# Kernel tuning notes

Hardware: AMD Instinct MI355X
Metric: run time of the kernel (lower is better)

The kernel has to match this reference:

```python
import jax, jax.numpy as jnp
import numpy as np

D_MODEL, N_LATENTS, D_LATENT, N_HEADS = 2048, 512, 1024, 16
D_H = D_LATENT // N_HEADS
B, N = 4, 4096


def _split_heads(x):
    b, t, _ = x.shape
    return x.reshape(b, t, N_HEADS, D_H).transpose(0, 2, 1, 3)  # [B,H,T,d_h]


def _merge_heads(x):
    b, h, t, d = x.shape
    return x.transpose(0, 2, 1, 3).reshape(b, t, h * d)


def _apply_rope(x, cos, sin):
    b, h, s, d = x.shape
    xr = x.reshape(b, h, s, d // 2, 2)
    x1, x2 = xr[..., 0], xr[..., 1]
    c = cos[:s][None, None]  # [1,1,s,d/2]
    sn = sin[:s][None, None]
    o1 = x1 * c - x2 * sn
    o2 = x1 * sn + x2 * c
    return jnp.stack([o1, o2], axis=-1).reshape(b, h, s, d)


def _attn(Q, K, V, causal=False, padding_mask=None):
    scale = 1.0 / np.sqrt(D_H).astype(np.float32)
    scores = jnp.einsum('bhqd,bhkd->bhqk', Q, K) * scale
    if causal:
        sq, sk = Q.shape[-2], K.shape[-2]
        causal_mask = jnp.triu(jnp.ones((sq, sk), dtype=bool), k=1)
        scores = jnp.where(causal_mask[None, None], -jnp.inf, scores)
    if padding_mask is not None:
        scores = jnp.where(padding_mask[:, None, None, :], -jnp.inf, scores)
    w = jax.nn.softmax(scores, axis=-1)
    w = jnp.nan_to_num(w, nan=0.0)
    return jnp.einsum('bhqk,bhkd->bhqd', w, V)


def setup_inputs() -> dict:
    key = jax.random.key(0)
    ks = jax.random.split(key, 10)
    x = jax.random.normal(ks[0], (B, N, D_MODEL), dtype=jnp.float32)
    # real RoPE cache (head_dim = D_H)
    half = D_H // 2
    inv_freq = 1.0 / (10000.0 ** (jnp.arange(half, dtype=jnp.float32) / half))
    angles = jnp.arange(N, dtype=jnp.float32)[:, None] * inv_freq[None, :]
    cos, sin = jnp.cos(angles), jnp.sin(angles)
    padding_mask = jnp.zeros((B, N), dtype=bool)
    s = 0.02
    L = jax.random.normal(ks[1], (N_LATENTS, D_LATENT), jnp.float32) * (D_LATENT ** -0.5)
    Wq_lat = jax.random.normal(ks[2], (D_LATENT, D_LATENT), jnp.float32) * s
    Wk_in = jax.random.normal(ks[3], (D_MODEL, D_LATENT), jnp.float32) * s
    Wv_in = jax.random.normal(ks[4], (D_MODEL, D_LATENT), jnp.float32) * s
    Wq_in = jax.random.normal(ks[5], (D_MODEL, D_LATENT), jnp.float32) * s
    Wk_lat = jax.random.normal(ks[6], (D_LATENT, D_LATENT), jnp.float32) * s
    Wv_lat = jax.random.normal(ks[7], (D_LATENT, D_LATENT), jnp.float32) * s
    Wout = jax.random.normal(ks[8], (D_LATENT, D_MODEL), jnp.float32) * s
    return {"x": x, "cos": cos, "sin": sin, "padding_mask": padding_mask,
            "L": L, "Wq_lat": Wq_lat, "Wk_in": Wk_in, "Wv_in": Wv_in,
            "Wq_in": Wq_in, "Wk_lat": Wk_lat, "Wv_lat": Wv_lat, "Wout": Wout}


def reference(x, cos, sin, padding_mask, L, Wq_lat, Wk_in, Wv_in, Wq_in, Wk_lat, Wv_lat, Wout):
    b = x.shape[0]
    Lb = jnp.broadcast_to(L[None], (b, N_LATENTS, D_LATENT))
    # stage 1: latents query inputs (causal + padding)
    Q = _split_heads(Lb @ Wq_lat)
    K = _apply_rope(_split_heads(x @ Wk_in), cos, sin)
    V = _split_heads(x @ Wv_in)
    z = _merge_heads(_attn(Q, K, V, causal=True, padding_mask=padding_mask))
    # stage 2: latent self-attention
    Ql = _split_heads(z @ Wq_lat)
    Kl = _split_heads(z @ Wk_lat)
    Vl = _split_heads(z @ Wv_lat)
    z2 = _merge_heads(_attn(Ql, Kl, Vl))
    # stage 3: inputs query latents
    Qx = _apply_rope(_split_heads(x @ Wq_in), cos, sin)
    Kz = _split_heads(z2 @ Wk_lat)
    Vz = _split_heads(z2 @ Wv_lat)
    x_latent = _merge_heads(_attn(Qx, Kz, Vz))
    return x_latent @ Wout
```

## Files before the change

kernel.cpp:

```cpp
#include <hip/hip_runtime.h>
#include <math.h>

#define D_MODEL 2048
#define N_LAT   512
#define D_LATENT 1024
#define N_HEADS 16
#define D_H 64
#define BATCH 4
#define SEQ 4096

typedef __attribute__((ext_vector_type(4))) float f32x4;
typedef __attribute__((ext_vector_type(8))) short short8;

__device__ inline ushort f2bf(float f) {
    uint u = __float_as_uint(f);
    uint r = (u + 0x7fffu + ((u >> 16) & 1u)) >> 16;
    return (ushort)r;
}
__device__ inline float bf2f(ushort h) { return __uint_as_float((uint)h << 16); }
__device__ inline uint pk(ushort a, ushort b) { return (uint)a | ((uint)b << 16); }

__global__ __launch_bounds__(256) void pack_w(
    const float* __restrict__ W, ushort* __restrict__ Ph, ushort* __restrict__ Pl,
    int K, int N)
{
    __shared__ float T[64][65];
    const int k0 = blockIdx.x * 64, n0 = blockIdx.y * 64;
    const int tid = threadIdx.x;
    for (int i = tid; i < 64 * 16; i += 256) {
        int kl = i >> 4, nc = (i & 15) * 4;
        float4 v = *(const float4*)(W + (long)(k0 + kl) * N + n0 + nc);
        T[kl][nc] = v.x; T[kl][nc + 1] = v.y; T[kl][nc + 2] = v.z; T[kl][nc + 3] = v.w;
    }
    __syncthreads();
    const int nl = tid >> 2, kc = (tid & 3) * 16;
    ushort h[16], l[16];
#pragma unroll
    for (int j = 0; j < 16; ++j) {
        float v = T[kc + j][nl];
        ushort hb = f2bf(v);
        float r = v - bf2f(hb);
        h[j] = hb; l[j] = f2bf(r);
    }
    long o = (long)(n0 + nl) * K + k0 + kc;
    *(uint4*)(Ph + o)     = make_uint4(pk(h[0],h[1]), pk(h[2],h[3]), pk(h[4],h[5]), pk(h[6],h[7]));
    *(uint4*)(Ph + o + 8) = make_uint4(pk(h[8],h[9]), pk(h[10],h[11]), pk(h[12],h[13]), pk(h[14],h[15]));
    *(uint4*)(Pl + o)     = make_uint4(pk(l[0],l[1]), pk(l[2],l[3]), pk(l[4],l[5]), pk(l[6],l[7]));
    *(uint4*)(Pl + o + 8) = make_uint4(pk(l[8],l[9]), pk(l[10],l[11]), pk(l[12],l[13]), pk(l[14],l[15]));
}

__global__ __launch_bounds__(256) void split2bf(
    const float* __restrict__ X, ushort* __restrict__ H, ushort* __restrict__ L, long n)
{
    long i = ((long)blockIdx.x * 256 + threadIdx.x) * 4;
    const long stride = (long)gridDim.x * 1024;
    for (; i < n; i += stride) {
        float4 v = *(const float4*)(X + i);
        ushort h0 = f2bf(v.x), h1 = f2bf(v.y), h2 = f2bf(v.z), h3 = f2bf(v.w);
        ushort l0 = f2bf(v.x - bf2f(h0)), l1 = f2bf(v.y - bf2f(h1)),
               l2 = f2bf(v.z - bf2f(h2)), l3 = f2bf(v.w - bf2f(h3));
        uint2 hw; hw.x = pk(h0, h1); hw.y = pk(h2, h3);
        uint2 lw; lw.x = pk(l0, l1); lw.y = pk(l2, l3);
        *(uint2*)(H + i) = hw;
        *(uint2*)(L + i) = lw;
    }
}

__global__ __launch_bounds__(512) void gemm_mfma8(
    const ushort* __restrict__ Ah, const ushort* __restrict__ Al,
    const ushort* __restrict__ Bh0, const ushort* __restrict__ Bl0,
    const ushort* __restrict__ Bh1, const ushort* __restrict__ Bl1,
    const ushort* __restrict__ Bh2, const ushort* __restrict__ Bl2,
    float* __restrict__ C0, float* __restrict__ C1, float* __restrict__ C2,
    int N, int K, long asb, long csb, int nMt)
{
    __shared__ ushort sAh[128][40], sAl[128][40];
    __shared__ ushort sBh[128][40], sBl[128][40];

    const int gx = gridDim.x;
    const int nblk = gx * gridDim.y;
    int bl = blockIdx.y * gx + blockIdx.x;
    if ((nblk & 7) == 0)
        bl = (bl & 7) * (nblk >> 3) + (bl >> 3);
    const int bx = bl % gx;
    const int by = bl / gx;

    const int wsel = by / nMt, mt0 = by % nMt;
    const ushort* Bh = (wsel == 0) ? Bh0 : ((wsel == 1) ? Bh1 : Bh2);
    const ushort* Bl = (wsel == 0) ? Bl0 : ((wsel == 1) ? Bl1 : Bl2);
    float* C = (wsel == 0) ? C0 : ((wsel == 1) ? C1 : C2);
    Ah += (long)blockIdx.z * asb;
    Al += (long)blockIdx.z * asb;
    C  += (long)blockIdx.z * csb;
    const int row0 = mt0 * 128, col0 = bx * 128;
    const int tid = threadIdx.x;
    const int lane = tid & 63, w = tid >> 6;
    const int wm = (w >> 2) * 64;
    const int wn = (w & 3) * 32;

    f32x4 acc[4][2];
#pragma unroll
    for (int i = 0; i < 4; ++i)
#pragma unroll
        for (int j = 0; j < 2; ++j) acc[i][j] = (f32x4)0.f;

    const int srow = tid >> 2;
    const int scol = (tid & 3) * 8;
    const ushort* Ahp = Ah + (long)(row0 + srow) * K + scol;
    const ushort* Alp = Al + (long)(row0 + srow) * K + scol;
    const ushort* Bhp = Bh + (long)(col0 + srow) * K + scol;
    const ushort* Blp = Bl + (long)(col0 + srow) * K + scol;

    const int fr = lane & 15, fk = (lane >> 4) * 8;

    for (int k0 = 0; k0 < K; k0 += 32) {
        uint4 ra_h = *(const uint4*)(Ahp + k0);
        uint4 ra_l = *(const uint4*)(Alp + k0);
        uint4 rb_h = *(const uint4*)(Bhp + k0);
        uint4 rb_l = *(const uint4*)(Blp + k0);
        __syncthreads();
        *(uint4*)&sAh[srow][scol] = ra_h;
        *(uint4*)&sAl[srow][scol] = ra_l;
        *(uint4*)&sBh[srow][scol] = rb_h;
        *(uint4*)&sBl[srow][scol] = rb_l;
        __syncthreads();

        short8 bhf[2], blf[2];
#pragma unroll
        for (int nt = 0; nt < 2; ++nt) {
            bhf[nt] = *(const short8*)&sBh[wn + nt * 16 + fr][fk];
            blf[nt] = *(const short8*)&sBl[wn + nt * 16 + fr][fk];
        }
#pragma unroll
        for (int mt = 0; mt < 4; ++mt) {
            short8 ah = *(const short8*)&sAh[wm + mt * 16 + fr][fk];
            short8 al = *(const short8*)&sAl[wm + mt * 16 + fr][fk];
#pragma unroll
            for (int nt = 0; nt < 2; ++nt) {
                acc[mt][nt] = __builtin_amdgcn_mfma_f32_16x16x32_bf16(al, bhf[nt], acc[mt][nt], 0, 0, 0);
                acc[mt][nt] = __builtin_amdgcn_mfma_f32_16x16x32_bf16(ah, blf[nt], acc[mt][nt], 0, 0, 0);
                acc[mt][nt] = __builtin_amdgcn_mfma_f32_16x16x32_bf16(ah, bhf[nt], acc[mt][nt], 0, 0, 0);
            }
        }
    }

    const int cr = (lane >> 4) * 4, cc = lane & 15;
#pragma unroll
    for (int mt = 0; mt < 4; ++mt)
#pragma unroll
        for (int nt = 0; nt < 2; ++nt) {
            float* cp = C + (long)(row0 + wm + mt * 16 + cr) * N + col0 + wn + nt * 16 + cc;
#pragma unroll
            for (int i = 0; i < 4; ++i) cp[(long)i * N] = acc[mt][nt][i];
        }
}

__global__ __launch_bounds__(512) void gemm_mfma8_f32a(
    const float* __restrict__ A,
    const ushort* __restrict__ Bh0, const ushort* __restrict__ Bl0,
    const ushort* __restrict__ Bh1, const ushort* __restrict__ Bl1,
    float* __restrict__ C0, float* __restrict__ C1,
    int N, int K, long asb, long csb, int nMt)
{
    __shared__ ushort sAh[128][40], sAl[128][40];
    __shared__ ushort sBh[128][40], sBl[128][40];

    const int gx = gridDim.x;
    const int nblk = gx * gridDim.y;
    int bl = blockIdx.y * gx + blockIdx.x;
    if ((nblk & 7) == 0)
        bl = (bl & 7) * (nblk >> 3) + (bl >> 3);
    const int bx = bl % gx;
    const int by = bl / gx;

    const int wsel = by / nMt, mt0 = by % nMt;
    const ushort* Bh = (wsel == 0) ? Bh0 : Bh1;
    const ushort* Bl = (wsel == 0) ? Bl0 : Bl1;
    float* C = (wsel == 0) ? C0 : C1;
    A += (long)blockIdx.z * asb;
    C += (long)blockIdx.z * csb;
    const int row0 = mt0 * 128, col0 = bx * 128;
    const int tid = threadIdx.x;
    const int lane = tid & 63, w = tid >> 6;
    const int wm = (w >> 2) * 64;
    const int wn = (w & 3) * 32;

    f32x4 acc[4][2];
#pragma unroll
    for (int i = 0; i < 4; ++i)
#pragma unroll
        for (int j = 0; j < 2; ++j) acc[i][j] = (f32x4)0.f;

    const int srow = tid >> 2;
    const int scol = (tid & 3) * 8;
    const float*  Ap  = A  + (long)(row0 + srow) * K + scol;
    const ushort* Bhp = Bh + (long)(col0 + srow) * K + scol;
    const ushort* Blp = Bl + (long)(col0 + srow) * K + scol;

    const int fr = lane & 15, fk = (lane >> 4) * 8;

    for (int k0 = 0; k0 < K; k0 += 32) {
        float4 a0 = *(const float4*)(Ap + k0);
        float4 a1 = *(const float4*)(Ap + k0 + 4);
        uint4 rb_h = *(const uint4*)(Bhp + k0);
        uint4 rb_l = *(const uint4*)(Blp + k0);
        uint4 wh, wl;
        {
            float v[8] = {a0.x, a0.y, a0.z, a0.w, a1.x, a1.y, a1.z, a1.w};
            ushort hh[8], ll[8];
#pragma unroll
            for (int j = 0; j < 8; ++j) {
                hh[j] = f2bf(v[j]);
                ll[j] = f2bf(v[j] - bf2f(hh[j]));
            }
            wh = make_uint4(pk(hh[0],hh[1]), pk(hh[2],hh[3]), pk(hh[4],hh[5]), pk(hh[6],hh[7]));
            wl = make_uint4(pk(ll[0],ll[1]), pk(ll[2],ll[3]), pk(ll[4],ll[5]), pk(ll[6],ll[7]));
        }
        __syncthreads();
        *(uint4*)&sAh[srow][scol] = wh;
        *(uint4*)&sAl[srow][scol] = wl;
        *(uint4*)&sBh[srow][scol] = rb_h;
        *(uint4*)&sBl[srow][scol] = rb_l;
        __syncthreads();

        short8 bhf[2], blf[2];
#pragma unroll
        for (int nt = 0; nt < 2; ++nt) {
            bhf[nt] = *(const short8*)&sBh[wn + nt * 16 + fr][fk];
            blf[nt] = *(const short8*)&sBl[wn + nt * 16 + fr][fk];
        }
#pragma unroll
        for (int mt = 0; mt < 4; ++mt) {
            short8 ah = *(const short8*)&sAh[wm + mt * 16 + fr][fk];
            short8 al = *(const short8*)&sAl[wm + mt * 16 + fr][fk];
#pragma unroll
            for (int nt = 0; nt < 2; ++nt) {
                acc[mt][nt] = __builtin_amdgcn_mfma_f32_16x16x32_bf16(al, bhf[nt], acc[mt][nt], 0, 0, 0);
                acc[mt][nt] = __builtin_amdgcn_mfma_f32_16x16x32_bf16(ah, blf[nt], acc[mt][nt], 0, 0, 0);
                acc[mt][nt] = __builtin_amdgcn_mfma_f32_16x16x32_bf16(ah, bhf[nt], acc[mt][nt], 0, 0, 0);
            }
        }
    }

    const int cr = (lane >> 4) * 4, cc = lane & 15;
#pragma unroll
    for (int mt = 0; mt < 4; ++mt)
#pragma unroll
        for (int nt = 0; nt < 2; ++nt) {
            float* cp = C + (long)(row0 + wm + mt * 16 + cr) * N + col0 + wn + nt * 16 + cc;
#pragma unroll
            for (int i = 0; i < 4; ++i) cp[(long)i * N] = acc[mt][nt][i];
        }
}

__global__ __launch_bounds__(256) void rope_f32(
    float* __restrict__ X, const float* __restrict__ cosT, const float* __restrict__ sinT,
    int S, int nb)
{
    long idx = (long)blockIdx.x * blockDim.x + threadIdx.x;
    long total = (long)nb * S * (D_LATENT / 2);
    if (idx >= total) return;
    int pair = (int)(idx & (D_LATENT / 2 - 1));
    long rs = idx >> 9;
    int s = (int)(rs % S);
    long b = rs / S;
    int h = pair >> 5, t = pair & 31;
    long base = (b * S + s) * (long)D_LATENT + h * D_H + 2 * t;
    float x1 = X[base], x2 = X[base + 1];
    float c = cosT[(long)s * 32 + t], sn = sinT[(long)s * 32 + t];
    X[base]     = x1 * c - x2 * sn;
    X[base + 1] = x1 * sn + x2 * c;
}

__global__ __launch_bounds__(256) void attn_mfma(
    const float* __restrict__ Q,
    const ushort* __restrict__ Kh, const ushort* __restrict__ Kl,
    const ushort* __restrict__ VTh, const ushort* __restrict__ VTl,
    ushort* __restrict__ Oh, ushort* __restrict__ Ol,
    long qbs, long kvbs, long obs)
{
    const int b = blockIdx.z, h = blockIdx.y;
    const int qb0 = blockIdx.x * 64;
    const float*  Qp  = Q   + (long)b * qbs + h * D_H;
    const ushort* Khp = Kh  + (long)b * kvbs + h * D_H;
    const ushort* Klp = Kl  + (long)b * kvbs + h * D_H;
    const ushort* VThp = VTh + (long)b * kvbs + (long)h * D_H * 512;
    const ushort* VTlp = VTl + (long)b * kvbs + (long)h * D_H * 512;
    ushort* Ohp = Oh + (long)b * obs + h * D_H;
    ushort* Olp = Ol + (long)b * obs + h * D_H;

    __shared__ ushort QVhs[64][72], QVls[64][72];
    __shared__ ushort Khs[64][72], Kls[64][72];
    __shared__ ushort Ps[4][16][72];

    const int tid = threadIdx.x;
    const int w = tid >> 6, lane = tid & 63;
    const int fr = lane & 15, g = lane >> 4, fk = g * 8;

    {
        const int q = tid >> 2, d0 = (tid & 3) * 16;
        const float* qrow = Qp + (long)(qb0 + q) * D_LATENT + d0;
#pragma unroll
        for (int c = 0; c < 4; ++c) {
            float4 v = *(const float4*)(qrow + 4 * c);
            ushort h0 = f2bf(v.x), h1 = f2bf(v.y), h2 = f2bf(v.z), h3 = f2bf(v.w);
            ushort l0 = f2bf(v.x - bf2f(h0)), l1 = f2bf(v.y - bf2f(h1)),
                   l2 = f2bf(v.z - bf2f(h2)), l3 = f2bf(v.w - bf2f(h3));
            uint2 hw; hw.x = pk(h0, h1); hw.y = pk(h2, h3);
            uint2 lw; lw.x = pk(l0, l1); lw.y = pk(l2, l3);
            *(uint2*)&QVhs[q][d0 + 4 * c] = hw;
            *(uint2*)&QVls[q][d0 + 4 * c] = lw;
        }
    }
    __syncthreads();

    const short8 qh0 = *(const short8*)&QVhs[w * 16 + fr][fk];
    const short8 qh1 = *(const short8*)&QVhs[w * 16 + fr][32 + fk];
    const short8 ql0 = *(const short8*)&QVls[w * 16 + fr][fk];
    const short8 ql1 = *(const short8*)&QVls[w * 16 + fr][32 + fk];

    f32x4 ot[4];
#pragma unroll
    for (int dt = 0; dt < 4; ++dt) ot[dt] = (f32x4)0.f;
    float mq = -1e30f, lq = 0.f;

    for (int kc = 0; kc < 512; kc += 64) {
        __syncthreads();
        {
            const int r = tid >> 2, cb = (tid & 3) * 16;
            const ushort* kh = Khp + (long)(kc + r) * D_LATENT + cb;
            const ushort* kl = Klp + (long)(kc + r) * D_LATENT + cb;
            const ushort* vh = VThp + (long)r * 512 + kc + cb;
            const ushort* vl = VTlp + (long)r * 512 + kc + cb;
            uint4 a0 = *(const uint4*)kh,       a1 = *(const uint4*)(kh + 8);
            uint4 b0 = *(const uint4*)kl,       b1 = *(const uint4*)(kl + 8);
            uint4 c0 = *(const uint4*)vh,       c1 = *(const uint4*)(vh + 8);
            uint4 d0v = *(const uint4*)vl,      d1v = *(const uint4*)(vl + 8);
            *(uint4*)&Khs[r][cb] = a0; *(uint4*)&Khs[r][cb + 8] = a1;
            *(uint4*)&Kls[r][cb] = b0; *(uint4*)&Kls[r][cb + 8] = b1;
            *(uint4*)&QVhs[r][cb] = c0; *(uint4*)&QVhs[r][cb + 8] = c1;
            *(uint4*)&QVls[r][cb] = d0v; *(uint4*)&QVls[r][cb + 8] = d1v;
        }
        __syncthreads();

        f32x4 sc[4];
#pragma unroll
        for (int t = 0; t < 4; ++t) {
            short8 kh0 = *(const short8*)&Khs[t * 16 + fr][fk];
            short8 kh1 = *(const short8*)&Khs[t * 16 + fr][32 + fk];
            short8 kl0 = *(const short8*)&Kls[t * 16 + fr][fk];
            short8 kl1 = *(const short8*)&Kls[t * 16 + fr][32 + fk];
            f32x4 a = (f32x4)0.f;
            a = __builtin_amdgcn_mfma_f32_16x16x32_bf16(kh0, ql0, a, 0, 0, 0);
            a = __builtin_amdgcn_mfma_f32_16x16x32_bf16(kh1, ql1, a, 0, 0, 0);
            a = __builtin_amdgcn_mfma_f32_16x16x32_bf16(kl0, qh0, a, 0, 0, 0);
            a = __builtin_amdgcn_mfma_f32_16x16x32_bf16(kl1, qh1, a, 0, 0, 0);
            a = __builtin_amdgcn_mfma_f32_16x16x32_bf16(kh0, qh0, a, 0, 0, 0);
            a = __builtin_amdgcn_mfma_f32_16x16x32_bf16(kh1, qh1, a, 0, 0, 0);
            sc[t] = a;
        }

        float cm = -1e30f;
#pragma unroll
        for (int t = 0; t < 4; ++t)
#pragma unroll
            for (int r = 0; r < 4; ++r) {
                sc[t][r] *= 0.125f;
                cm = fmaxf(cm, sc[t][r]);
            }
        cm = fmaxf(cm, __shfl_xor(cm, 16));
        cm = fmaxf(cm, __shfl_xor(cm, 32));
        const float mnew = fmaxf(mq, cm);
        const float alpha = __expf(mq - mnew);
        float tsum = 0.f;
#pragma unroll
        for (int t = 0; t < 4; ++t)
#pragma unroll
            for (int r = 0; r < 4; ++r) {
                float p = __expf(sc[t][r] - mnew);
                sc[t][r] = p;
                tsum += p;
            }
        tsum += __shfl_xor(tsum, 16);
        tsum += __shfl_xor(tsum, 32);
        lq = lq * alpha + tsum;
        mq = mnew;
#pragma unroll
        for (int dt = 0; dt < 4; ++dt) ot[dt] = ot[dt] * alpha;

#pragma unroll
        for (int t = 0; t < 4; ++t)
#pragma unroll
            for (int r = 0; r < 4; ++r)
                Ps[w][fr][t * 16 + g * 4 + r] = f2bf(sc[t][r]);

#pragma unroll
        for (int ks = 0; ks < 2; ++ks) {
            short8 bp = *(const short8*)&Ps[w][fr][ks * 32 + fk];
#pragma unroll
            for (int dt = 0; dt < 4; ++dt) {
                short8 avh = *(const short8*)&QVhs[dt * 16 + fr][ks * 32 + fk];
                short8 avl = *(const short8*)&QVls[dt * 16 + fr][ks * 32 + fk];
                ot[dt] = __builtin_amdgcn_mfma_f32_16x16x32_bf16(avh, bp, ot[dt], 0, 0, 0);
                ot[dt] = __builtin_amdgcn_mfma_f32_16x16x32_bf16(avl, bp, ot[dt], 0, 0, 0);
            }
        }
    }

    __syncthreads();
    const float inv = 1.0f / lq;
#pragma unroll
    for (int dt = 0; dt < 4; ++dt)
#pragma unroll
        for (int r = 0; r < 4; ++r) {
            float v = ot[dt][r] * inv;
            ushort hb = f2bf(v);
            Khs[w * 16 + fr][dt * 16 + g * 4 + r] = hb;
            Kls[w * 16 + fr][dt * 16 + g * 4 + r] = f2bf(v - bf2f(hb));
        }
    __syncthreads();
    {
        const int q = tid >> 2, d0 = (tid & 3) * 16;
        ushort* oh = Ohp + (long)(qb0 + q) * D_LATENT + d0;
        ushort* ol = Olp + (long)(qb0 + q) * D_LATENT + d0;
        *(uint4*)oh       = *(const uint4*)&Khs[q][d0];
        *(uint4*)(oh + 8) = *(const uint4*)&Khs[q][d0 + 8];
        *(uint4*)ol       = *(const uint4*)&Kls[q][d0];
        *(uint4*)(ol + 8) = *(const uint4*)&Kls[q][d0 + 8];
    }
}

#define ABQ 64
#define ABK 64
#define APAD 68

__global__ __launch_bounds__(256, 3) void attn_f32(
    const float* __restrict__ Q, const float* __restrict__ K, const float* __restrict__ V,
    ushort* __restrict__ Oh, ushort* __restrict__ Ol,
    int Sq, int Sk, long qbs, long kvbs, long obs, int causal)
{
    const int b = blockIdx.z, h = blockIdx.y;
    const int qb0 = blockIdx.x * ABQ;
    const float* Qp = Q + (long)b * qbs + h * D_H;
    const float* Kp = K + (long)b * kvbs + h * D_H;
    const float* Vp = V + (long)b * kvbs + h * D_H;
    ushort* Ohp = Oh + (long)b * obs + h * D_H;
    ushort* Olp = Ol + (long)b * obs + h * D_H;

    __shared__ float Qs[D_H][APAD];
    __shared__ float KPs[D_H][APAD];
    __shared__ float Vs[ABK][APAD];

    const int tid = threadIdx.x;
    const int tm = tid >> 4;
    const int tn = tid & 15;
    const int q4 = tm * 4, n4 = tn * 4;

    for (int i = tid; i < ABQ * 16; i += 256) {
        int q = i >> 4, d0 = (i & 15) * 4;
        float4 t = *(const float4*)(Qp + (long)(qb0 + q) * D_LATENT + d0);
        Qs[d0 + 0][q] = t.x; Qs[d0 + 1][q] = t.y; Qs[d0 + 2][q] = t.z; Qs[d0 + 3][q] = t.w;
    }

    float o[4][4], mq[4], lq[4];
#pragma unroll
    for (int i = 0; i < 4; ++i) {
        mq[i] = -1e30f; lq[i] = 0.f;
#pragma unroll
        for (int j = 0; j < 4; ++j) o[i][j] = 0.f;
    }

    const int kend = causal ? min(Sk, qb0 + ABQ) : Sk;

    for (int kc = 0; kc < kend; kc += ABK) {
        __syncthreads();
        for (int i = tid; i < ABK * 16; i += 256) {
            int k = i >> 4, d0 = (i & 15) * 4;
            float4 kt = *(const float4*)(Kp + (long)(kc + k) * D_LATENT + d0);
            KPs[d0 + 0][k] = kt.x; KPs[d0 + 1][k] = kt.y; KPs[d0 + 2][k] = kt.z; KPs[d0 + 3][k] = kt.w;
            float4 vt = *(const float4*)(Vp + (long)(kc + k) * D_LATENT + d0);
            *(float4*)&Vs[k][d0] = vt;
        }
        __syncthreads();

        float s[4][4];
#pragma unroll
        for (int qi = 0; qi < 4; ++qi)
#pragma unroll
            for (int kj = 0; kj < 4; ++kj) s[qi][kj] = 0.f;

#pragma unroll 4
        for (int d = 0; d < D_H; ++d) {
            float4 qv = *(const float4*)&Qs[d][q4];
            float4 kv = *(const float4*)&KPs[d][n4];
            float qa[4] = {qv.x, qv.y, qv.z, qv.w};
            float ka[4] = {kv.x, kv.y, kv.z, kv.w};
#pragma unroll
            for (int qi = 0; qi < 4; ++qi)
#pragma unroll
                for (int kj = 0; kj < 4; ++kj) s[qi][kj] += qa[qi] * ka[kj];
        }
        __syncthreads();

        const bool diag = (causal != 0) && (kc + ABK > qb0);
#pragma unroll
        for (int qi = 0; qi < 4; ++qi) {
            const int gq = qb0 + q4 + qi;
#pragma unroll
            for (int kj = 0; kj < 4; ++kj) {
                float sv = s[qi][kj] * 0.125f;
                if (diag && (kc + n4 + kj > gq)) sv = -1e30f;
                s[qi][kj] = sv;
            }
            float cm = fmaxf(fmaxf(s[qi][0], s[qi][1]), fmaxf(s[qi][2], s[qi][3]));
#pragma unroll
            for (int off = 8; off; off >>= 1) cm = fmaxf(cm, __shfl_xor(cm, off));
            const float mnew = fmaxf(mq[qi], cm);
            float ps = 0.f;
#pragma unroll
            for (int kj = 0; kj < 4; ++kj) {
                float p = __expf(s[qi][kj] - mnew);
                s[qi][kj] = p;
                ps += p;
            }
#pragma unroll
            for (int off = 8; off; off >>= 1) ps += __shfl_xor(ps, off);
            const float alpha = __expf(mq[qi] - mnew);
            lq[qi] = lq[qi] * alpha + ps;
            mq[qi] = mnew;
#pragma unroll
            for (int dj = 0; dj < 4; ++dj) o[qi][dj] *= alpha;
        }
#pragma unroll
        for (int kj = 0; kj < 4; ++kj)
            *(float4*)&KPs[n4 + kj][q4] = make_float4(s[0][kj], s[1][kj], s[2][kj], s[3][kj]);
        __syncthreads();

#pragma unroll 4
        for (int k = 0; k < ABK; ++k) {
            float4 pv = *(const float4*)&KPs[k][q4];
            float4 vv = *(const float4*)&Vs[k][n4];
            float pa[4] = {pv.x, pv.y, pv.z, pv.w};
            float va[4] = {vv.x, vv.y, vv.z, vv.w};
#pragma unroll
            for (int qi = 0; qi < 4; ++qi)
#pragma unroll
                for (int dj = 0; dj < 4; ++dj) o[qi][dj] += pa[qi] * va[dj];
        }
    }

#pragma unroll
    for (int qi = 0; qi < 4; ++qi) {
        const float inv = 1.0f / lq[qi];
        float v0 = o[qi][0] * inv, v1 = o[qi][1] * inv, v2 = o[qi][2] * inv, v3 = o[qi][3] * inv;
        ushort h0 = f2bf(v0), h1 = f2bf(v1), h2 = f2bf(v2), h3 = f2bf(v3);
        ushort l0 = f2bf(v0 - bf2f(h0)), l1 = f2bf(v1 - bf2f(h1)),
               l2 = f2bf(v2 - bf2f(h2)), l3 = f2bf(v3 - bf2f(h3));
        uint2 hw; hw.x = pk(h0, h1); hw.y = pk(h2, h3);
        uint2 lw; lw.x = pk(l0, l1); lw.y = pk(l2, l3);
        long off = (long)(qb0 + q4 + qi) * D_LATENT + n4;
        *(uint2*)(Ohp + off) = hw;
        *(uint2*)(Olp + off) = lw;
    }
}

extern "C" void kernel_launch(void* const* d_in, const int* in_sizes, int n_in,
                              void* d_out, int out_size, void* d_ws, size_t ws_size,
                              hipStream_t stream)
{
    const float* x     = (const float*)d_in[0];
    const float* cosT  = (const float*)d_in[1];
    const float* sinT  = (const float*)d_in[2];
    const float* L      = (const float*)d_in[4];
    const float* Wq_lat = (const float*)d_in[5];
    const float* Wk_in  = (const float*)d_in[6];
    const float* Wv_in  = (const float*)d_in[7];
    const float* Wq_in  = (const float*)d_in[8];
    const float* Wk_lat = (const float*)d_in[9];
    const float* Wv_lat = (const float*)d_in[10];
    const float* Wout   = (const float*)d_in[11];
    float* out = (float*)d_out;
    float* ws  = (float*)d_ws;
    ushort* wsu = (ushort*)d_ws;
    ushort* ob  = (ushort*)d_out;

    const long F  = 524288;
    const long UU = 1048576;
    if (ws_size < (size_t)47 * UU * 2) return;

    ushort *Po_h  = wsu + 0 * UU, *Po_l  = wsu + 2 * UU;
    ushort *Pqi_h = wsu + 4 * UU, *Pqi_l = wsu + 6 * UU;
    ushort *Pql_h = wsu + 8 * UU, *Pql_l = wsu + 9 * UU;
    ushort *Pki_h = wsu + 10 * UU, *Pki_l = wsu + 12 * UU;
    ushort *Pvi_h = wsu + 14 * UU, *Pvi_l = wsu + 16 * UU;
    ushort *Pkl_h = wsu + 18 * UU, *Pkl_l = wsu + 19 * UU;
    ushort *Pvl_h = wsu + 20 * UU, *Pvl_l = wsu + 21 * UU;
    float  *Q1 = ws + 31 * F;
    float  *K1 = ws + 32 * F, *V1 = ws + 36 * F;
    ushort *zh = wsu + 40 * UU, *zl = wsu + 42 * UU;
    float  *Ql = ws + 23 * F, *Kl = ws + 27 * F, *Vl = ws + 32 * F;
    ushort *Klh = wsu + 40 * UU, *Kll = wsu + 42 * UU;
    ushort *VlTh = wsu + 27 * UU, *VlTl = wsu + 29 * UU;
    ushort *z2h = wsu + 36 * UU, *z2l = wsu + 38 * UU;
    float  *Kz = ws + 23 * F, *Vz = ws + 27 * F;
    ushort *Kzh = wsu + 31 * UU, *Kzl = wsu + 33 * UU;
    ushort *VzTh = wsu + 35 * UU, *VzTl = wsu + 37 * UU;
    ushort *xl23h = wsu + 22 * UU;
    ushort *xl23l = wsu + 39 * UU;

    float  *Qx = out;
    ushort *xl01h = ob + 32 * UU, *xl01l = ob + 40 * UU;

    dim3 blk(256), blk5(512);
    const long SB = (long)N_LAT * D_LATENT;
    const long XB = (long)SEQ * D_MODEL;
    const long QB = (long)SEQ * D_LATENT;

    pack_w<<<dim3(16, 32), blk, 0, stream>>>(Wout,   Po_h,  Po_l,  1024, 2048);
    pack_w<<<dim3(32, 16), blk, 0, stream>>>(Wq_in,  Pqi_h, Pqi_l, 2048, 1024);
    pack_w<<<dim3(16, 16), blk, 0, stream>>>(Wq_lat, Pql_h, Pql_l, 1024, 1024);
    pack_w<<<dim3(32, 16), blk, 0, stream>>>(Wk_in,  Pki_h, Pki_l, 2048, 1024);
    pack_w<<<dim3(32, 16), blk, 0, stream>>>(Wv_in,  Pvi_h, Pvi_l, 2048, 1024);
    pack_w<<<dim3(16, 16), blk, 0, stream>>>(Wk_lat, Pkl_h, Pkl_l, 1024, 1024);
    pack_w<<<dim3(16, 16), blk, 0, stream>>>(Wv_lat, Pvl_h, Pvl_l, 1024, 1024);

    gemm_mfma8_f32a<<<dim3(8, 4, 1), blk5, 0, stream>>>(
        L, Pql_h, Pql_l, nullptr, nullptr,
        Q1, nullptr, 1024, 1024, 0L, 0L, 4);
    gemm_mfma8_f32a<<<dim3(8, 8, BATCH), blk5, 0, stream>>>(
        x, Pki_h, Pki_l, Pvi_h, Pvi_l,
        K1, V1, 1024, 2048, (long)SEQ * D_MODEL, SB, 4);
    {
        long total = (long)BATCH * N_LAT * (D_LATENT / 2);
        rope_f32<<<dim3((unsigned)((total + 255) / 256)), blk, 0, stream>>>(K1, cosT, sinT, N_LAT, BATCH);
    }
    attn_f32<<<dim3(N_LAT / ABQ, N_HEADS, BATCH), blk, 0, stream>>>(
        Q1, K1, V1, zh, zl, N_LAT, N_LAT, 0L, SB, SB, 1);

    gemm_mfma8<<<dim3(8, 12, BATCH), blk5, 0, stream>>>(
        zh, zl, Pql_h, Pql_l, Pkl_h, Pkl_l, Pvl_h, Pvl_l,
        Ql, Kl, Vl, 1024, 1024, SB, SB, 4);
    split2bf<<<dim3(512), blk, 0, stream>>>(Kl, Klh, Kll, 4L * SB);
    for (int b = 0; b < BATCH; ++b)
        pack_w<<<dim3(8, 16), blk, 0, stream>>>(
            Vl + (long)b * SB, VlTh + (long)b * SB, VlTl + (long)b * SB, 512, 1024);
    attn_mfma<<<dim3(N_LAT / 64, N_HEADS, BATCH), blk, 0, stream>>>(
        Ql, Klh, Kll, VlTh, VlTl, z2h, z2l, SB, SB, SB);

    gemm_mfma8<<<dim3(8, 8, BATCH), blk5, 0, stream>>>(
        z2h, z2l, Pkl_h, Pkl_l, Pvl_h, Pvl_l, nullptr, nullptr,
        Kz, Vz, nullptr, 1024, 1024, SB, SB, 4);
    split2bf<<<dim3(512), blk, 0, stream>>>(Kz, Kzh, Kzl, 4L * SB);
    for (int b = 0; b < BATCH; ++b)
        pack_w<<<dim3(8, 16), blk, 0, stream>>>(
            Vz + (long)b * SB, VzTh + (long)b * SB, VzTl + (long)b * SB, 512, 1024);

    gemm_mfma8_f32a<<<dim3(8, 64, 1), blk5, 0, stream>>>(
        x, Pqi_h, Pqi_l, nullptr, nullptr,
        Qx, nullptr, 1024, 2048, 0L, 0L, 64);
    gemm_mfma8_f32a<<<dim3(8, 64, 1), blk5, 0, stream>>>(
        x + 2L * XB, Pqi_h, Pqi_l, nullptr, nullptr,
        Qx + 2L * QB, nullptr, 1024, 2048, 0L, 0L, 64);
    {
        long total = (long)BATCH * SEQ * (D_LATENT / 2);
        rope_f32<<<dim3((unsigned)((total + 255) / 256)), blk, 0, stream>>>(Qx, cosT, sinT, SEQ, BATCH);
    }
    attn_mfma<<<dim3(SEQ / 64, N_HEADS, 2), blk, 0, stream>>>(
        Qx, Kzh, Kzl, VzTh, VzTl, xl01h, xl01l, QB, SB, QB);
    attn_mfma<<<dim3(SEQ / 64, N_HEADS, 2), blk, 0, stream>>>(
        Qx + 2L * QB, Kzh + 2L * SB, Kzl + 2L * SB, VzTh + 2L * SB, VzTl + 2L * SB,
        xl23h, xl23l, QB, SB, QB);
    gemm_mfma8<<<dim3(16, 64, 1), blk5, 0, stream>>>(
        xl01h, xl01l, Po_h, Po_l, nullptr, nullptr, nullptr, nullptr,
        out, nullptr, nullptr, 2048, 1024, 0L, 0L, 64);
    gemm_mfma8<<<dim3(16, 64, 1), blk5, 0, stream>>>(
        xl23h, xl23l, Po_h, Po_l, nullptr, nullptr, nullptr, nullptr,
        out + 2L * SEQ * D_MODEL, nullptr, nullptr, 2048, 1024, 0L, 0L, 64);
}
```

Before: 1.048 ms.

## Use MFMA attention for causal stage and smaller GEMM tiles for latent GEMMs

The scalar fp32 stage-1 attention is replaced by the MFMA split-bf16 attention kernel, which gains a causal flag with diagonal masking and early loop termination. K1 is split into bf16 hi/lo parts and V1 is transposed to feed it. The GEMM kernels are templated on M-tile size, so the small latent GEMMs run with 64-row tiles for more blocks, and the two Qx GEMM launches are merged into one. The costs are extra split and pack passes, and lower per-block reuse in the smaller-tile GEMMs.

After: 967.6 us. 7.7% less time.

```diff
diff --git a/kernel.cpp b/kernel.cpp
--- a/kernel.cpp
+++ b/kernel.cpp
@@ -66,6 +66,7 @@
     }
 }
 
+template<int MT>
 __global__ __launch_bounds__(512) void gemm_mfma8(
     const ushort* __restrict__ Ah, const ushort* __restrict__ Al,
     const ushort* __restrict__ Bh0, const ushort* __restrict__ Bl0,
@@ -74,7 +75,8 @@
     float* __restrict__ C0, float* __restrict__ C1, float* __restrict__ C2,
     int N, int K, long asb, long csb, int nMt)
 {
-    __shared__ ushort sAh[128][40], sAl[128][40];
+    constexpr int BM = MT * 32;
+    __shared__ ushort sAh[BM][40], sAl[BM][40];
     __shared__ ushort sBh[128][40], sBl[128][40];
 
     const int gx = gridDim.x;
@@ -92,37 +94,47 @@
     Ah += (long)blockIdx.z * asb;
     Al += (long)blockIdx.z * asb;
     C  += (long)blockIdx.z * csb;
-    const int row0 = mt0 * 128, col0 = bx * 128;
+    const int row0 = mt0 * BM, col0 = bx * 128;
     const int tid = threadIdx.x;
     const int lane = tid & 63, w = tid >> 6;
-    const int wm = (w >> 2) * 64;
+    const int wm = (w >> 2) * (MT * 16);
     const int wn = (w & 3) * 32;
 
-    f32x4 acc[4][2];
-#pragma unroll
-    for (int i = 0; i < 4; ++i)
+    f32x4 acc[MT][2];
+#pragma unroll
+    for (int i = 0; i < MT; ++i)
 #pragma unroll
         for (int j = 0; j < 2; ++j) acc[i][j] = (f32x4)0.f;
 
-    const int srow = tid >> 2;
-    const int scol = (tid & 3) * 8;
-    const ushort* Ahp = Ah + (long)(row0 + srow) * K + scol;
-    const ushort* Alp = Al + (long)(row0 + srow) * K + scol;
-    const ushort* Bhp = Bh + (long)(col0 + srow) * K + scol;
-    const ushort* Blp = Bl + (long)(col0 + srow) * K + scol;
+    const int srA = (MT == 4) ? (tid >> 2) : (tid >> 3);
+    const int scA = (MT == 4) ? ((tid & 3) * 8) : ((tid & 7) * 4);
+    const int srB = tid >> 2;
+    const int scB = (tid & 3) * 8;
+    const ushort* Ahp = Ah + (long)(row0 + srA) * K + scA;
+    const ushort* Alp = Al + (long)(row0 + srA) * K + scA;
+    const ushort* Bhp = Bh + (long)(col0 + srB) * K + scB;
+    const ushort* Blp = Bl + (long)(col0 + srB) * K + scB;
 
     const int fr = lane & 15, fk = (lane >> 4) * 8;
 
     for (int k0 = 0; k0 < K; k0 += 32) {
-        uint4 ra_h = *(const uint4*)(Ahp + k0);
-        uint4 ra_l = *(const uint4*)(Alp + k0);
         uint4 rb_h = *(const uint4*)(Bhp + k0);
         uint4 rb_l = *(const uint4*)(Blp + k0);
-        __syncthreads();
-        *(uint4*)&sAh[srow][scol] = ra_h;
-        *(uint4*)&sAl[srow][scol] = ra_l;
-        *(uint4*)&sBh[srow][scol] = rb_h;
-        *(uint4*)&sBl[srow][scol] = rb_l;
+        if constexpr (MT == 4) {
+            uint4 ra_h = *(const uint4*)(Ahp + k0);
+            uint4 ra_l = *(const uint4*)(Alp + k0);
+            __syncthreads();
+            *(uint4*)&sAh[srA][scA] = ra_h;
+            *(uint4*)&sAl[srA][scA] = ra_l;
+        } else {
+            uint2 ra_h = *(const uint2*)(Ahp + k0);
+            uint2 ra_l = *(const uint2*)(Alp + k0);
+            __syncthreads();
+            *(uint2*)&sAh[srA][scA] = ra_h;
+            *(uint2*)&sAl[srA][scA] = ra_l;
+        }
+        *(uint4*)&sBh[srB][scB] = rb_h;
+        *(uint4*)&sBl[srB][scB] = rb_l;
         __syncthreads();
 
         short8 bhf[2], blf[2];
@@ -132,7 +144,7 @@
             blf[nt] = *(const short8*)&sBl[wn + nt * 16 + fr][fk];
         }
 #pragma unroll
-        for (int mt = 0; mt < 4; ++mt) {
+        for (int mt = 0; mt < MT; ++mt) {
             short8 ah = *(const short8*)&sAh[wm + mt * 16 + fr][fk];
             short8 al = *(const short8*)&sAl[wm + mt * 16 + fr][fk];
 #pragma unroll
@@ -146,7 +158,7 @@
 
     const int cr = (lane >> 4) * 4, cc = lane & 15;
 #pragma unroll
-    for (int mt = 0; mt < 4; ++mt)
+    for (int mt = 0; mt < MT; ++mt)
 #pragma unroll
         for (int nt = 0; nt < 2; ++nt) {
             float* cp = C + (long)(row0 + wm + mt * 16 + cr) * N + col0 + wn + nt * 16 + cc;
@@ -155,6 +167,7 @@
         }
 }
 
+template<int MT>
 __global__ __launch_bounds__(512) void gemm_mfma8_f32a(
     const float* __restrict__ A,
     const ushort* __restrict__ Bh0, const ushort* __restrict__ Bl0,
@@ -162,7 +175,8 @@
     float* __restrict__ C0, float* __restrict__ C1,
     int N, int K, long asb, long csb, int nMt)
 {
-    __shared__ ushort sAh[128][40], sAl[128][40];
+    constexpr int BM = MT * 32;
+    __shared__ ushort sAh[BM][40], sAl[BM][40];
     __shared__ ushort sBh[128][40], sBl[128][40];
 
     const int gx = gridDim.x;
@@ -179,48 +193,69 @@
     float* C = (wsel == 0) ? C0 : C1;
     A += (long)blockIdx.z * asb;
     C += (long)blockIdx.z * csb;
-    const int row0 = mt0 * 128, col0 = bx * 128;
+    const int row0 = mt0 * BM, col0 = bx * 128;
     const int tid = threadIdx.x;
     const int lane = tid & 63, w = tid >> 6;
-    const int wm = (w >> 2) * 64;
+    const int wm = (w >> 2) * (MT * 16);
     const int wn = (w & 3) * 32;
 
-    f32x4 acc[4][2];
-#pragma unroll
-    for (int i = 0; i < 4; ++i)
+    f32x4 acc[MT][2];
+#pragma unroll
+    for (int i = 0; i < MT; ++i)
 #pragma unroll
         for (int j = 0; j < 2; ++j) acc[i][j] = (f32x4)0.f;
 
-    const int srow = tid >> 2;
-    const int scol = (tid & 3) * 8;
-    const float*  Ap  = A  + (long)(row0 + srow) * K + scol;
-    const ushort* Bhp = Bh + (long)(col0 + srow) * K + scol;
-    const ushort* Blp = Bl + (long)(col0 + srow) * K + scol;
+    const int srA = (MT == 4) ? (tid >> 2) : (tid >> 3);
+    const int scA = (MT == 4) ? ((tid & 3) * 8) : ((tid & 7) * 4);
+    const int srB = tid >> 2;
+    const int scB = (tid & 3) * 8;
+    const float*  Ap  = A  + (long)(row0 + srA) * K + scA;
+    const ushort* Bhp = Bh + (long)(col0 + srB) * K + scB;
+    const ushort* Blp = Bl + (long)(col0 + srB) * K + scB;
 
     const int fr = lane & 15, fk = (lane >> 4) * 8;
 
     for (int k0 = 0; k0 < K; k0 += 32) {
-        float4 a0 = *(const float4*)(Ap + k0);
-        float4 a1 = *(const float4*)(Ap + k0 + 4);
         uint4 rb_h = *(const uint4*)(Bhp + k0);
         uint4 rb_l = *(const uint4*)(Blp + k0);
-        uint4 wh, wl;
-        {
-            float v[8] = {a0.x, a0.y, a0.z, a0.w, a1.x, a1.y, a1.z, a1.w};
-            ushort hh[8], ll[8];
-#pragma unroll
-            for (int j = 0; j < 8; ++j) {
-                hh[j] = f2bf(v[j]);
-                ll[j] = f2bf(v[j] - bf2f(hh[j]));
-            }
-            wh = make_uint4(pk(hh[0],hh[1]), pk(hh[2],hh[3]), pk(hh[4],hh[5]), pk(hh[6],hh[7]));
-            wl = make_uint4(pk(ll[0],ll[1]), pk(ll[2],ll[3]), pk(ll[4],ll[5]), pk(ll[6],ll[7]));
-        }
-        __syncthreads();
-        *(uint4*)&sAh[srow][scol] = wh;
-        *(uint4*)&sAl[srow][scol] = wl;
-        *(uint4*)&sBh[srow][scol] = rb_h;
-        *(uint4*)&sBl[srow][scol] = rb_l;
+        if constexpr (MT == 4) {
+            float4 a0 = *(const float4*)(Ap + k0);
+            float4 a1 = *(const float4*)(Ap + k0 + 4);
+            uint4 wh, wl;
+            {
+                float v[8] = {a0.x, a0.y, a0.z, a0.w, a1.x, a1.y, a1.z, a1.w};
+                ushort hh[8], ll[8];
+#pragma unroll
+                for (int j = 0; j < 8; ++j) {
+                    hh[j] = f2bf(v[j]);
+                    ll[j] = f2bf(v[j] - bf2f(hh[j]));
+                }
+                wh = make_uint4(pk(hh[0],hh[1]), pk(hh[2],hh[3]), pk(hh[4],hh[5]), pk(hh[6],hh[7]));
+                wl = make_uint4(pk(ll[0],ll[1]), pk(ll[2],ll[3]), pk(ll[4],ll[5]), pk(ll[6],ll[7]));
+            }
+            __syncthreads();
+            *(uint4*)&sAh[srA][scA] = wh;
+            *(uint4*)&sAl[srA][scA] = wl;
+        } else {
+            float4 a0 = *(const float4*)(Ap + k0);
+            uint2 wh, wl;
+            {
+                float v[4] = {a0.x, a0.y, a0.z, a0.w};
+                ushort hh[4], ll[4];
+#pragma unroll
+                for (int j = 0; j < 4; ++j) {
+                    hh[j] = f2bf(v[j]);
+                    ll[j] = f2bf(v[j] - bf2f(hh[j]));
+                }
+                wh.x = pk(hh[0], hh[1]); wh.y = pk(hh[2], hh[3]);
+                wl.x = pk(ll[0], ll[1]); wl.y = pk(ll[2], ll[3]);
+            }
+            __syncthreads();
+            *(uint2*)&sAh[srA][scA] = wh;
+            *(uint2*)&sAl[srA][scA] = wl;
+        }
+        *(uint4*)&sBh[srB][scB] = rb_h;
+        *(uint4*)&sBl[srB][scB] = rb_l;
         __syncthreads();
 
         short8 bhf[2], blf[2];
@@ -230,7 +265,7 @@
             blf[nt] = *(const short8*)&sBl[wn + nt * 16 + fr][fk];
         }
 #pragma unroll
-        for (int mt = 0; mt < 4; ++mt) {
+        for (int mt = 0; mt < MT; ++mt) {
             short8 ah = *(const short8*)&sAh[wm + mt * 16 + fr][fk];
             short8 al = *(const short8*)&sAl[wm + mt * 16 + fr][fk];
 #pragma unroll
@@ -244,7 +279,7 @@
 
     const int cr = (lane >> 4) * 4, cc = lane & 15;
 #pragma unroll
-    for (int mt = 0; mt < 4; ++mt)
+    for (int mt = 0; mt < MT; ++mt)
 #pragma unroll
         for (int nt = 0; nt < 2; ++nt) {
             float* cp = C + (long)(row0 + wm + mt * 16 + cr) * N + col0 + wn + nt * 16 + cc;
@@ -277,7 +312,7 @@
     const ushort* __restrict__ Kh, const ushort* __restrict__ Kl,
     const ushort* __restrict__ VTh, const ushort* __restrict__ VTl,
     ushort* __restrict__ Oh, ushort* __restrict__ Ol,
-    long qbs, long kvbs, long obs)
+    long qbs, long kvbs, long obs, int causal)
 {
     const int b = blockIdx.z, h = blockIdx.y;
     const int qb0 = blockIdx.x * 64;
@@ -324,7 +359,9 @@
     for (int dt = 0; dt < 4; ++dt) ot[dt] = (f32x4)0.f;
     float mq = -1e30f, lq = 0.f;
 
-    for (int kc = 0; kc < 512; kc += 64) {
+    const int kend = causal ? (qb0 + 64) : 512;
+
+    for (int kc = 0; kc < kend; kc += 64) {
         __syncthreads();
         {
             const int r = tid >> 2, cb = (tid & 3) * 16;
@@ -360,13 +397,16 @@
             sc[t] = a;
         }
 
+        const bool diag = (causal != 0) && (kc + 64 > qb0);
         float cm = -1e30f;
 #pragma unroll
         for (int t = 0; t < 4; ++t)
 #pragma unroll
             for (int r = 0; r < 4; ++r) {
-                sc[t][r] *= 0.125f;
-                cm = fmaxf(cm, sc[t][r]);
+                float sv = sc[t][r] * 0.125f;
+                if (diag && (kc + t * 16 + g * 4 + r > qb0 + w * 16 + fr)) sv = -1e30f;
+                sc[t][r] = sv;
+                cm = fmaxf(cm, sv);
             }
         cm = fmaxf(cm, __shfl_xor(cm, 16));
         cm = fmaxf(cm, __shfl_xor(cm, 32));
@@ -427,140 +467,6 @@
         *(uint4*)(oh + 8) = *(const uint4*)&Khs[q][d0 + 8];
         *(uint4*)ol       = *(const uint4*)&Kls[q][d0];
         *(uint4*)(ol + 8) = *(const uint4*)&Kls[q][d0 + 8];
-    }
-}
-
-#define ABQ 64
-#define ABK 64
-#define APAD 68
-
-__global__ __launch_bounds__(256, 3) void attn_f32(
-    const float* __restrict__ Q, const float* __restrict__ K, const float* __restrict__ V,
-    ushort* __restrict__ Oh, ushort* __restrict__ Ol,
-    int Sq, int Sk, long qbs, long kvbs, long obs, int causal)
-{
-    const int b = blockIdx.z, h = blockIdx.y;
-    const int qb0 = blockIdx.x * ABQ;
-    const float* Qp = Q + (long)b * qbs + h * D_H;
-    const float* Kp = K + (long)b * kvbs + h * D_H;
-    const float* Vp = V + (long)b * kvbs + h * D_H;
-    ushort* Ohp = Oh + (long)b * obs + h * D_H;
-    ushort* Olp = Ol + (long)b * obs + h * D_H;
-
-    __shared__ float Qs[D_H][APAD];
-    __shared__ float KPs[D_H][APAD];
-    __shared__ float Vs[ABK][APAD];
-
-    const int tid = threadIdx.x;
-    const int tm = tid >> 4;
-    const int tn = tid & 15;
-    const int q4 = tm * 4, n4 = tn * 4;
-
-    for (int i = tid; i < ABQ * 16; i += 256) {
-        int q = i >> 4, d0 = (i & 15) * 4;
-        float4 t = *(const float4*)(Qp + (long)(qb0 + q) * D_LATENT + d0);
-        Qs[d0 + 0][q] = t.x; Qs[d0 + 1][q] = t.y; Qs[d0 + 2][q] = t.z; Qs[d0 + 3][q] = t.w;
-    }
-
-    float o[4][4], mq[4], lq[4];
-#pragma unroll
-    for (int i = 0; i < 4; ++i) {
-        mq[i] = -1e30f; lq[i] = 0.f;
-#pragma unroll
-        for (int j = 0; j < 4; ++j) o[i][j] = 0.f;
-    }
-
-    const int kend = causal ? min(Sk, qb0 + ABQ) : Sk;
-
-    for (int kc = 0; kc < kend; kc += ABK) {
-        __syncthreads();
-        for (int i = tid; i < ABK * 16; i += 256) {
-            int k = i >> 4, d0 = (i & 15) * 4;
-            float4 kt = *(const float4*)(Kp + (long)(kc + k) * D_LATENT + d0);
-            KPs[d0 + 0][k] = kt.x; KPs[d0 + 1][k] = kt.y; KPs[d0 + 2][k] = kt.z; KPs[d0 + 3][k] = kt.w;
-            float4 vt = *(const float4*)(Vp + (long)(kc + k) * D_LATENT + d0);
-            *(float4*)&Vs[k][d0] = vt;
-        }
-        __syncthreads();
-
-        float s[4][4];
-#pragma unroll
-        for (int qi = 0; qi < 4; ++qi)
-#pragma unroll
-            for (int kj = 0; kj < 4; ++kj) s[qi][kj] = 0.f;
-
-#pragma unroll 4
-        for (int d = 0; d < D_H; ++d) {
-            float4 qv = *(const float4*)&Qs[d][q4];
-            float4 kv = *(const float4*)&KPs[d][n4];
-            float qa[4] = {qv.x, qv.y, qv.z, qv.w};
-            float ka[4] = {kv.x, kv.y, kv.z, kv.w};
-#pragma unroll
-            for (int qi = 0; qi < 4; ++qi)
-#pragma unroll
-                for (int kj = 0; kj < 4; ++kj) s[qi][kj] += qa[qi] * ka[kj];
-        }
-        __syncthreads();
-
-        const bool diag = (causal != 0) && (kc + ABK > qb0);
-#pragma unroll
-        for (int qi = 0; qi < 4; ++qi) {
-            const int gq = qb0 + q4 + qi;
-#pragma unroll
-            for (int kj = 0; kj < 4; ++kj) {
-                float sv = s[qi][kj] * 0.125f;
-                if (diag && (kc + n4 + kj > gq)) sv = -1e30f;
-                s[qi][kj] = sv;
-            }
-            float cm = fmaxf(fmaxf(s[qi][0], s[qi][1]), fmaxf(s[qi][2], s[qi][3]));
-#pragma unroll
-            for (int off = 8; off; off >>= 1) cm = fmaxf(cm, __shfl_xor(cm, off));
-            const float mnew = fmaxf(mq[qi], cm);
-            float ps = 0.f;
-#pragma unroll
-            for (int kj = 0; kj < 4; ++kj) {
-                float p = __expf(s[qi][kj] - mnew);
-                s[qi][kj] = p;
-                ps += p;
-            }
-#pragma unroll
-            for (int off = 8; off; off >>= 1) ps += __shfl_xor(ps, off);
-            const float alpha = __expf(mq[qi] - mnew);
-            lq[qi] = lq[qi] * alpha + ps;
-            mq[qi] = mnew;
-#pragma unroll
-            for (int dj = 0; dj < 4; ++dj) o[qi][dj] *= alpha;
-        }
-#pragma unroll
-        for (int kj = 0; kj < 4; ++kj)
-            *(float4*)&KPs[n4 + kj][q4] = make_float4(s[0][kj], s[1][kj], s[2][kj], s[3][kj]);
-        __syncthreads();
-
-#pragma unroll 4
-        for (int k = 0; k < ABK; ++k) {
-            float4 pv = *(const float4*)&KPs[k][q4];
-            float4 vv = *(const float4*)&Vs[k][n4];
-            float pa[4] = {pv.x, pv.y, pv.z, pv.w};
-            float va[4] = {vv.x, vv.y, vv.z, vv.w};
-#pragma unroll
-            for (int qi = 0; qi < 4; ++qi)
-#pragma unroll
-                for (int dj = 0; dj < 4; ++dj) o[qi][dj] += pa[qi] * va[dj];
-        }
-    }
-
-#pragma unroll
-    for (int qi = 0; qi < 4; ++qi) {
-        const float inv = 1.0f / lq[qi];
-        float v0 = o[qi][0] * inv, v1 = o[qi][1] * inv, v2 = o[qi][2] * inv, v3 = o[qi][3] * inv;
-        ushort h0 = f2bf(v0), h1 = f2bf(v1), h2 = f2bf(v2), h3 = f2bf(v3);
-        ushort l0 = f2bf(v0 - bf2f(h0)), l1 = f2bf(v1 - bf2f(h1)),
-               l2 = f2bf(v2 - bf2f(h2)), l3 = f2bf(v3 - bf2f(h3));
-        uint2 hw; hw.x = pk(h0, h1); hw.y = pk(h2, h3);
-        uint2 lw; lw.x = pk(l0, l1); lw.y = pk(l2, l3);
-        long off = (long)(qb0 + q4 + qi) * D_LATENT + n4;
-        *(uint2*)(Ohp + off) = hw;
-        *(uint2*)(Olp + off) = lw;
     }
 }
 
@@ -597,6 +503,8 @@
     ushort *Pvl_h = wsu + 20 * UU, *Pvl_l = wsu + 21 * UU;
     float  *Q1 = ws + 31 * F;
     float  *K1 = ws + 32 * F, *V1 = ws + 36 * F;
+    ushort *K1h = wsu + 22 * UU, *K1l = wsu + 24 * UU;
+    ushort *V1Th = wsu + 26 * UU, *V1Tl = wsu + 28 * UU;
     ushort *zh = wsu + 40 * UU, *zl = wsu + 42 * UU;
     float  *Ql = ws + 23 * F, *Kl = ws + 27 * F, *Vl = ws + 32 * F;
     ushort *Klh = wsu + 40 * UU, *Kll = wsu + 42 * UU;
@@ -624,56 +532,57 @@
     pack_w<<<dim3(16, 16), blk, 0, stream>>>(Wk_lat, Pkl_h, Pkl_l, 1024, 1024);
     pack_w<<<dim3(16, 16), blk, 0, stream>>>(Wv_lat, Pvl_h, Pvl_l, 1024, 1024);
 
-    gemm_mfma8_f32a<<<dim3(8, 4, 1), blk5, 0, stream>>>(
+    gemm_mfma8_f32a<2><<<dim3(8, 8, 1), blk5, 0, stream>>>(
         L, Pql_h, Pql_l, nullptr, nullptr,
-        Q1, nullptr, 1024, 1024, 0L, 0L, 4);
-    gemm_mfma8_f32a<<<dim3(8, 8, BATCH), blk5, 0, stream>>>(
+        Q1, nullptr, 1024, 1024, 0L, 0L, 8);
+    gemm_mfma8_f32a<2><<<dim3(8, 16, BATCH), blk5, 0, stream>>>(
         x, Pki_h, Pki_l, Pvi_h, Pvi_l,
-        K1, V1, 1024, 2048, (long)SEQ * D_MODEL, SB, 4);
+        K1, V1, 1024, 2048, (long)SEQ * D_MODEL, SB, 8);
     {
         long total = (long)BATCH * N_LAT * (D_LATENT / 2);
         rope_f32<<<dim3((unsigned)((total + 255) / 256)), blk, 0, stream>>>(K1, cosT, sinT, N_LAT, BATCH);
     }
-    attn_f32<<<dim3(N_LAT / ABQ, N_HEADS, BATCH), blk, 0, stream>>>(
-        Q1, K1, V1, zh, zl, N_LAT, N_LAT, 0L, SB, SB, 1);
-
-    gemm_mfma8<<<dim3(8, 12, BATCH), blk5, 0, stream>>>(
+    split2bf<<<dim3(512), blk, 0, stream>>>(K1, K1h, K1l, 4L * SB);
+    for (int b = 0; b < BATCH; ++b)
+        pack_w<<<dim3(8, 16), blk, 0, stream>>>(
+            V1 + (long)b * SB, V1Th + (long)b * SB, V1Tl + (long)b * SB, 512, 1024);
+    attn_mfma<<<dim3(N_LAT / 64, N_HEADS, BATCH), blk, 0, stream>>>(
+        Q1, K1h, K1l, V1Th, V1Tl, zh, zl, 0L, SB, SB, 1);
+
+    gemm_mfma8<2><<<dim3(8, 24, BATCH), blk5, 0, stream>>>(
         zh, zl, Pql_h, Pql_l, Pkl_h, Pkl_l, Pvl_h, Pvl_l,
-        Ql, Kl, Vl, 1024, 1024, SB, SB, 4);
+        Ql, Kl, Vl, 1024, 1024, SB, SB, 8);
     split2bf<<<dim3(512), blk, 0, stream>>>(Kl, Klh, Kll, 4L * SB);
     for (int b = 0; b < BATCH; ++b)
         pack_w<<<dim3(8, 16), blk, 0, stream>>>(
             Vl + (long)b * SB, VlTh + (long)b * SB, VlTl + (long)b * SB, 512, 1024);
     attn_mfma<<<dim3(N_LAT / 64, N_HEADS, BATCH), blk, 0, stream>>>(
-        Ql, Klh, Kll, VlTh, VlTl, z2h, z2l, SB, SB, SB);
-
-    gemm_mfma8<<<dim3(8, 8, BATCH), blk5, 0, stream>>>(
+        Ql, Klh, Kll, VlTh, VlTl, z2h, z2l, SB, SB, SB, 0);
+
+    gemm_mfma8<2><<<dim3(8, 16, BATCH), blk5, 0, stream>>>(
         z2h, z2l, Pkl_h, Pkl_l, Pvl_h, Pvl_l, nullptr, nullptr,
-        Kz, Vz, nullptr, 1024, 1024, SB, SB, 4);
+        Kz, Vz, nullptr, 1024, 1024, SB, SB, 8);
     split2bf<<<dim3(512), blk, 0, stream>>>(Kz, Kzh, Kzl, 4L * SB);
     for (int b = 0; b < BATCH; ++b)
         pack_w<<<dim3(8, 16), blk, 0, stream>>>(
             Vz + (long)b * SB, VzTh + (long)b * SB, VzTl + (long)b * SB, 512, 1024);
 
-    gemm_mfma8_f32a<<<dim3(8, 64, 1), blk5, 0, stream>>>(
+    gemm_mfma8_f32a<4><<<dim3(8, 128, 1), blk5, 0, stream>>>(
         x, Pqi_h, Pqi_l, nullptr, nullptr,
-        Qx, nullptr, 1024, 2048, 0L, 0L, 64);
-    gemm_mfma8_f32a<<<dim3(8, 64, 1), blk5, 0, stream>>>(
-        x + 2L * XB, Pqi_h, Pqi_l, nullptr, nullptr,
-        Qx + 2L * QB, nullptr, 1024, 2048, 0L, 0L, 64);
+        Qx, nullptr, 1024, 2048, 0L, 0L, 128);
     {
         long total = (long)BATCH * SEQ * (D_LATENT / 2);
         rope_f32<<<dim3((unsigned)((total + 255) / 256)), blk, 0, stream>>>(Qx, cosT, sinT, SEQ, BATCH);
     }
     attn_mfma<<<dim3(SEQ / 64, N_HEADS, 2), blk, 0, stream>>>(
-        Qx, Kzh, Kzl, VzTh, VzTl, xl01h, xl01l, QB, SB, QB);
+        Qx, Kzh, Kzl, VzTh, VzTl, xl01h, xl01l, QB, SB, QB, 0);
     attn_mfma<<<dim3(SEQ / 64, N_HEADS, 2), blk, 0, stream>>>(
         Qx + 2L * QB, Kzh + 2L * SB, Kzl + 2L * SB, VzTh + 2L * SB, VzTl + 2L * SB,
-        xl23h, xl23l, QB, SB, QB);
-    gemm_mfma8<<<dim3(16, 64, 1), blk5, 0, stream>>>(
+        xl23h, xl23l, QB, SB, QB, 0);
+    gemm_mfma8<4><<<dim3(16, 64, 1), blk5, 0, stream>>>(
         xl01h, xl01l, Po_h, Po_l, nullptr, nullptr, nullptr, nullptr,
         out, nullptr, nullptr, 2048, 1024, 0L, 0L, 64);
-    gemm_mfma8<<<dim3(16, 64, 1), blk5, 0, stream>>>(
+    gemm_mfma8<4><<<dim3(16, 64, 1), blk5, 0, stream>>>(
         xl23h, xl23l, Po_h, Po_l, nullptr, nullptr, nullptr, nullptr,
         out + 2L * SEQ * D_MODEL, nullptr, nullptr, 2048, 1024, 0L, 0L, 64);
 }
```
